# Optimization experiments

Hardware: AMD Instinct MI355X
Metric: run time of the kernel (lower is better)

## Reference

```python
import jax, jax.numpy as jnp
import numpy as np

DIM = 256
CODEBOOK_SIZE = 1024
CODEBOOK_DIM = 1024
COMMITMENT_COST = 1.0
CODEBOOK_COST = 0.25
LN_EPS = 1e-5


def setup_inputs() -> dict:
    key = jax.random.key(0)
    ks = jax.random.split(key, 6)
    x = jax.random.normal(ks[0], (4, 8192, DIM), dtype=jnp.float32)
    ln_gamma = jnp.ones((DIM,), jnp.float32)
    ln_beta = jnp.zeros((DIM,), jnp.float32)
    # pre_proj Linear(dim -> codebook_dim), stored as (in, out)
    pre_w = jax.random.normal(ks[1], (DIM, CODEBOOK_DIM), jnp.float32) / np.sqrt(DIM)
    pre_b = jnp.zeros((CODEBOOK_DIM,), jnp.float32)
    # codebook: unit-norm rows scaled by sqrt(codebook_dim)
    e = jax.random.normal(ks[2], (CODEBOOK_SIZE, CODEBOOK_DIM), jnp.float32)
    embed = e / jnp.linalg.norm(e, axis=1, keepdims=True) * np.sqrt(CODEBOOK_DIM)
    # post_proj Linear(codebook_dim -> dim)
    post_w = jax.random.normal(ks[3], (CODEBOOK_DIM, DIM), jnp.float32) / np.sqrt(CODEBOOK_DIM)
    post_b = jnp.zeros((DIM,), jnp.float32)
    return {"x": x, "ln_gamma": ln_gamma, "ln_beta": ln_beta,
            "pre_w": pre_w, "pre_b": pre_b, "embed": embed,
            "post_w": post_w, "post_b": post_b}


def _layer_norm(x, g, b):
    mu = jnp.mean(x, axis=-1, keepdims=True)
    var = jnp.mean(jnp.square(x - mu), axis=-1, keepdims=True)
    return (x - mu) * jax.lax.rsqrt(var + LN_EPS) * g + b


def reference(x, ln_gamma, ln_beta, pre_w, pre_b, embed, post_w, post_b):
    B, N, D = x.shape
    sg = jax.lax.stop_gradient
    # pre_norm -> GELU -> pre_proj
    x_normed = _layer_norm(x, ln_gamma, ln_beta)
    z_e = jax.nn.gelu(x_normed, approximate=False) @ pre_w + pre_b  # (B,N,Dc)
    flat = z_e.reshape(-1, CODEBOOK_DIM)  # (BN, Dc)
    # squared L2 distances to codebook: ||z||^2 - 2 z.E^T + ||e||^2
    z_sq = jnp.sum(flat * flat, axis=1, keepdims=True)        # (BN,1)
    e_sq = jnp.sum(embed * embed, axis=1)                      # (K,)
    dist = z_sq - 2.0 * (flat @ embed.T) + e_sq[None, :]       # (BN,K)
    indices = jnp.argmin(dist, axis=1)                          # (BN,)
    z_q = embed[indices]                                        # (BN,Dc)
    # losses
    codebook_loss = CODEBOOK_COST * jnp.mean(jnp.square(sg(flat) - z_q))
    commitment_loss = COMMITMENT_COST * jnp.mean(jnp.square(flat - sg(z_q)))
    vq_loss = codebook_loss + commitment_loss
    # straight-through estimator + post projection
    z_q_st = flat + sg(z_q - flat)
    quantized = (z_q_st.reshape(B, N, CODEBOOK_DIM)) @ post_w + post_b  # (B,N,D)
    return quantized, indices.reshape(B, N), vq_loss
```

## Files before the change

kernel.cpp:

```cpp
#include <hip/hip_runtime.h>
#include <math.h>

typedef __attribute__((ext_vector_type(8))) short short8;
typedef __attribute__((ext_vector_type(4))) float f32x4;

__device__ __forceinline__ unsigned short f2bf(float f) {
  unsigned u = __float_as_uint(f);
  unsigned r = (u + 0x7FFFu + ((u >> 16) & 1u)) >> 16;
  return (unsigned short)r;
}

__device__ __forceinline__ float bf2f(unsigned short u) {
  return __uint_as_float((unsigned)u << 16);
}

__device__ __forceinline__ void gload_lds16(const void* gsrc, void* ldst) {
  __builtin_amdgcn_global_load_lds(
      (__attribute__((address_space(1))) void*)(void*)(size_t)(const char*)gsrc,
      (__attribute__((address_space(3))) void*)ldst, 16, 0, 0);
}

__global__ __launch_bounds__(512) void prep1_kernel(
    const float* __restrict__ x, const float* __restrict__ ln_g,
    const float* __restrict__ ln_b, const float* __restrict__ pre_w,
    const float* __restrict__ pre_b, const float* __restrict__ embed,
    const float* __restrict__ post_w, const float* __restrict__ post_b,
    float* __restrict__ g, unsigned short* __restrict__ gbf,
    float* __restrict__ wtf, float* __restrict__ e_sq,
    float* __restrict__ qv, float* __restrict__ c0,
    float* __restrict__ eproj) {
  __shared__ __align__(16) char smem[16640];
  const int blk = blockIdx.x;
  const int t = threadIdx.x;
  if (blk < 256) {
    float (*Es)[1024] = (float(*)[1024])smem;
    const int k0 = blk * 4;
    *(float4*)(&Es[0][0] + t * 8) = *(const float4*)(embed + (size_t)k0 * 1024 + t * 8);
    *(float4*)(&Es[0][0] + t * 8 + 4) = *(const float4*)(embed + (size_t)k0 * 1024 + t * 8 + 4);
    __syncthreads();
    const int sl = t >> 6, jg = t & 63;
    const int dbase = sl * 128;
    float4 a[4] = {};
    const float* wp = post_w + (size_t)dbase * 256 + jg * 4;
#pragma unroll 8
    for (int dd = 0; dd < 128; ++dd) {
      float4 w4 = *(const float4*)(wp + (size_t)dd * 256);
      int d = dbase + dd;
#pragma unroll
      for (int kk = 0; kk < 4; ++kk) {
        float e = Es[kk][d];
        a[kk].x += w4.x * e; a[kk].y += w4.y * e;
        a[kk].z += w4.z * e; a[kk].w += w4.w * e;
      }
    }
    __syncthreads();
    float* scr = (float*)smem;
    if (sl >= 4)
#pragma unroll
      for (int kk = 0; kk < 4; ++kk)
        *(float4*)(scr + (sl - 4) * 1024 + kk * 256 + jg * 4) = a[kk];
    __syncthreads();
    if (sl < 4)
#pragma unroll
      for (int kk = 0; kk < 4; ++kk) {
        float4 v = *(const float4*)(scr + sl * 1024 + kk * 256 + jg * 4);
        a[kk].x += v.x; a[kk].y += v.y; a[kk].z += v.z; a[kk].w += v.w;
      }
    __syncthreads();
    if (sl >= 2 && sl < 4)
#pragma unroll
      for (int kk = 0; kk < 4; ++kk)
        *(float4*)(scr + (sl - 2) * 1024 + kk * 256 + jg * 4) = a[kk];
    __syncthreads();
    if (sl < 2)
#pragma unroll
      for (int kk = 0; kk < 4; ++kk) {
        float4 v = *(const float4*)(scr + sl * 1024 + kk * 256 + jg * 4);
        a[kk].x += v.x; a[kk].y += v.y; a[kk].z += v.z; a[kk].w += v.w;
      }
    __syncthreads();
    if (sl == 1)
#pragma unroll
      for (int kk = 0; kk < 4; ++kk)
        *(float4*)(scr + kk * 256 + jg * 4) = a[kk];
    __syncthreads();
    if (sl == 0) {
      float4 pb = *(const float4*)(post_b + jg * 4);
#pragma unroll
      for (int kk = 0; kk < 4; ++kk) {
        float4 v = *(const float4*)(scr + kk * 256 + jg * 4);
        float4 o;
        o.x = a[kk].x + v.x + pb.x;
        o.y = a[kk].y + v.y + pb.y;
        o.z = a[kk].z + v.z + pb.z;
        o.w = a[kk].w + v.w + pb.w;
        *(float4*)(eproj + (size_t)(k0 + kk) * 256 + jg * 4) = o;
      }
    }
  } else if (blk < 320) {
    float (*tile)[65] = (float(*)[65])smem;
    const int b = blk - 256;
    const int bc = b & 15, bd = b >> 4;
    const int col = t & 63, rr = t >> 6;
#pragma unroll
    for (int i = 0; i < 8; ++i) {
      int row = rr + i * 8;
      tile[row][col] = pre_w[(size_t)(bd * 64 + row) * 1024 + bc * 64 + col];
    }
    __syncthreads();
#pragma unroll
    for (int i = 0; i < 8; ++i) {
      int row = rr + i * 8;
      wtf[(size_t)(bc * 64 + row) * 256 + bd * 64 + col] = tile[col][row];
    }
  } else if (blk < 448) {
    const int l = t & 63, w = t >> 6;
    const int k = (blk - 320) * 8 + w;
    const float* er = embed + (size_t)k * 1024;
    float s1 = 0.f, s2 = 0.f;
#pragma unroll
    for (int j = 0; j < 16; ++j) {
      float e = er[l + 64 * j];
      s1 += e * e;
      s2 += pre_b[l + 64 * j] * e;
    }
    for (int m = 32; m; m >>= 1) { s1 += __shfl_xor(s1, m); s2 += __shfl_xor(s2, m); }
    if (l == 0) { e_sq[k] = s1; qv[k] = s2; c0[k] = s1 - 2.0f * s2 - 1024.0f; }
  } else {
    const int l = t & 63, w = t >> 6;
    const int r = (blk - 448) * 8 + w;
    const float4 xv = *(const float4*)(x + (size_t)r * 256 + l * 4);
    float s = xv.x + xv.y + xv.z + xv.w;
    for (int m = 32; m; m >>= 1) s += __shfl_xor(s, m);
    const float mu = s * (1.0f / 256.0f);
    float dx = xv.x - mu, dy = xv.y - mu, dz = xv.z - mu, dw = xv.w - mu;
    float vs = dx * dx + dy * dy + dz * dz + dw * dw;
    for (int m = 32; m; m >>= 1) vs += __shfl_xor(vs, m);
    const float rstd = rsqrtf(vs * (1.0f / 256.0f) + 1e-5f);
    float4 gm = *(const float4*)(ln_g + l * 4);
    float4 bt = *(const float4*)(ln_b + l * 4);
    float v0 = dx * rstd * gm.x + bt.x;
    float v1 = dy * rstd * gm.y + bt.y;
    float v2 = dz * rstd * gm.z + bt.z;
    float v3 = dw * rstd * gm.w + bt.w;
    const float is2 = 0.70710678118654752f;
    float4 o;
    o.x = 0.5f * v0 * (1.0f + erff(v0 * is2));
    o.y = 0.5f * v1 * (1.0f + erff(v1 * is2));
    o.z = 0.5f * v2 * (1.0f + erff(v2 * is2));
    o.w = 0.5f * v3 * (1.0f + erff(v3 * is2));
    *(float4*)(g + (size_t)r * 256 + l * 4) = o;
    ushort4 u;
    u.x = f2bf(o.x); u.y = f2bf(o.y); u.z = f2bf(o.z); u.w = f2bf(o.w);
    *(ushort4*)(gbf + (size_t)r * 256 + l * 4) = u;
  }
}

__global__ __launch_bounds__(512) void prep2_kernel(
    const float* __restrict__ embed, const float* __restrict__ pre_w,
    const float* __restrict__ pre_b, const float* __restrict__ wtf,
    float* __restrict__ prow, unsigned short* __restrict__ prowbf,
    unsigned short* __restrict__ qbf, float* __restrict__ wbv) {
  __shared__ __align__(16) char smem[49152];
  const int t = threadIdx.x;
  const int sl = t >> 6, jg = t & 63;
  if (blockIdx.x < 256) {
    float (*Es)[1024] = (float(*)[1024])smem;
    double (*Pd)[1024] = (double(*)[1024])(smem + 16384);
    const int k0 = blockIdx.x * 4;
    *(float4*)(&Es[0][0] + t * 8) = *(const float4*)(embed + (size_t)k0 * 1024 + t * 8);
    *(float4*)(&Es[0][0] + t * 8 + 4) = *(const float4*)(embed + (size_t)k0 * 1024 + t * 8 + 4);
    __syncthreads();
    const int cbase = sl * 128;
    double a[4][4] = {};
    const float* wp = wtf + (size_t)cbase * 256 + jg * 4;
#pragma unroll 8
    for (int cc = 0; cc < 128; ++cc) {
      float4 w4 = *(const float4*)(wp + (size_t)cc * 256);
      int c = cbase + cc;
#pragma unroll
      for (int kk = 0; kk < 4; ++kk) {
        double e = (double)Es[kk][c];
        a[kk][0] += (double)w4.x * e;
        a[kk][1] += (double)w4.y * e;
        a[kk][2] += (double)w4.z * e;
        a[kk][3] += (double)w4.w * e;
      }
    }
    if (sl >= 4)
#pragma unroll
      for (int kk = 0; kk < 4; ++kk)
#pragma unroll
        for (int xx = 0; xx < 4; ++xx) Pd[sl - 4][kk * 256 + jg * 4 + xx] = a[kk][xx];
    __syncthreads();
    if (sl < 4)
#pragma unroll
      for (int kk = 0; kk < 4; ++kk)
#pragma unroll
        for (int xx = 0; xx < 4; ++xx) a[kk][xx] += Pd[sl][kk * 256 + jg * 4 + xx];
    __syncthreads();
    if (sl >= 2 && sl < 4)
#pragma unroll
      for (int kk = 0; kk < 4; ++kk)
#pragma unroll
        for (int xx = 0; xx < 4; ++xx) Pd[sl - 2][kk * 256 + jg * 4 + xx] = a[kk][xx];
    __syncthreads();
    if (sl < 2)
#pragma unroll
      for (int kk = 0; kk < 4; ++kk)
#pragma unroll
        for (int xx = 0; xx < 4; ++xx) a[kk][xx] += Pd[sl][kk * 256 + jg * 4 + xx];
    __syncthreads();
    if (sl == 1)
#pragma unroll
      for (int kk = 0; kk < 4; ++kk)
#pragma unroll
        for (int xx = 0; xx < 4; ++xx) Pd[0][kk * 256 + jg * 4 + xx] = a[kk][xx];
    __syncthreads();
    if (sl == 0) {
#pragma unroll
      for (int kk = 0; kk < 4; ++kk) {
        float4 o;
        o.x = (float)(a[kk][0] + Pd[0][kk * 256 + jg * 4 + 0]);
        o.y = (float)(a[kk][1] + Pd[0][kk * 256 + jg * 4 + 1]);
        o.z = (float)(a[kk][2] + Pd[0][kk * 256 + jg * 4 + 2]);
        o.w = (float)(a[kk][3] + Pd[0][kk * 256 + jg * 4 + 3]);
        *(float4*)(prow + (size_t)(k0 + kk) * 256 + jg * 4) = o;
        ushort4 u;
        u.x = f2bf(o.x); u.y = f2bf(o.y); u.z = f2bf(o.z); u.w = f2bf(o.w);
        *(ushort4*)(prowbf + (size_t)(k0 + kk) * 256 + jg * 4) = u;
      }
    }
  } else if (blockIdx.x < 320) {
    float (*Es)[1024] = (float(*)[1024])smem;
    float (*Ps)[1024] = (float(*)[1024])(smem + 16384);
    const int a0i = (blockIdx.x - 256) * 4;
    *(float4*)(&Es[0][0] + t * 8) = *(const float4*)(pre_w + (size_t)a0i * 1024 + t * 8);
    *(float4*)(&Es[0][0] + t * 8 + 4) = *(const float4*)(pre_w + (size_t)a0i * 1024 + t * 8 + 4);
    __syncthreads();
    const int cbase = sl * 128;
    float4 a[4] = {};
    const float* wp = wtf + (size_t)cbase * 256 + jg * 4;
#pragma unroll 8
    for (int cc = 0; cc < 128; ++cc) {
      float4 w4 = *(const float4*)(wp + (size_t)cc * 256);
      int c = cbase + cc;
#pragma unroll
      for (int kk = 0; kk < 4; ++kk) {
        float e = Es[kk][c];
        a[kk].x += w4.x * e; a[kk].y += w4.y * e;
        a[kk].z += w4.z * e; a[kk].w += w4.w * e;
      }
    }
#pragma unroll
    for (int kk = 0; kk < 4; ++kk)
      *(float4*)(&Ps[sl][kk * 256 + jg * 4]) = a[kk];
    __syncthreads();
#pragma unroll
    for (int rep = 0; rep < 2; ++rep) {
      int o = t + rep * 512;
      float s = Ps[0][o] + Ps[1][o] + Ps[2][o] + Ps[3][o] +
                Ps[4][o] + Ps[5][o] + Ps[6][o] + Ps[7][o];
      int kk = o >> 8, j = o & 255;
      qbf[(size_t)(a0i + kk) * 256 + j] = f2bf(s);
    }
  } else {
    float* Es0 = (float*)smem;
    float (*Ps)[1024] = (float(*)[1024])(smem + 16384);
    const int cbase = sl * 128;
    float4 a = {0.f, 0.f, 0.f, 0.f};
    const float* wp = wtf + (size_t)cbase * 256 + jg * 4;
#pragma unroll 8
    for (int cc = 0; cc < 128; ++cc) {
      float4 w4 = *(const float4*)(wp + (size_t)cc * 256);
      float b = pre_b[cbase + cc];
      a.x += w4.x * b; a.y += w4.y * b; a.z += w4.z * b; a.w += w4.w * b;
    }
    *(float4*)(&Ps[sl][jg * 4]) = a;
    float sb = 0.f;
    if (t < 256) {
      float4 bv = *(const float4*)(pre_b + t * 4);
      sb = bv.x * bv.x + bv.y * bv.y + bv.z * bv.z + bv.w * bv.w;
    }
    for (int m = 32; m; m >>= 1) sb += __shfl_xor(sb, m);
    if ((t & 63) == 0 && t < 256) Es0[t >> 6] = sb;
    __syncthreads();
    if (t < 256) {
      float s = Ps[0][t] + Ps[1][t] + Ps[2][t] + Ps[3][t] +
                Ps[4][t] + Ps[5][t] + Ps[6][t] + Ps[7][t];
      wbv[t] = 2.f * s;
    }
    if (t == 0) wbv[256] = Es0[0] + Es0[1] + Es0[2] + Es0[3];
  }
}

__device__ __forceinline__ void stage_tile256(
    int t, const unsigned short* __restrict__ Asrc, size_t a_row_stride,
    const unsigned short* __restrict__ Bsrc, size_t b_row_stride, int k0,
    unsigned short* Ab, unsigned short* Bb) {
#pragma unroll
  for (int i = 0; i < 4; ++i) {
    int ca = t + 256 * i;
    int r = ca >> 3;
    int sp = (ca & 7) ^ (r & 7);
    gload_lds16(Asrc + (size_t)r * a_row_stride + k0 + sp * 8, (char*)Ab + ca * 16);
    gload_lds16(Bsrc + (size_t)r * b_row_stride + k0 + sp * 8, (char*)Bb + ca * 16);
  }
}

#define SAFE_LOOP_BODY(cur)                                                    \
    const unsigned short* Ab = &lds[cur][0];                                   \
    const unsigned short* Bb = &lds[cur][8192];                                \
    _Pragma("unroll")                                                          \
    for (int ks = 0; ks < 2; ++ks) {                                           \
      const int sp = ((ks << 2) + (l >> 4)) ^ (l & 7);                         \
      short8 af[4], bq[4];                                                     \
      _Pragma("unroll")                                                        \
      for (int mi = 0; mi < 4; ++mi)                                           \
        af[mi] = *(const short8*)(Ab + (wm + mi * 16 + (l & 15)) * 64 + sp * 8); \
      _Pragma("unroll")                                                        \
      for (int ni = 0; ni < 4; ++ni)                                           \
        bq[ni] = *(const short8*)(Bb + (wn + ni * 16 + (l & 15)) * 64 + sp * 8); \
      _Pragma("unroll")                                                        \
      for (int mi = 0; mi < 4; ++mi)                                           \
        _Pragma("unroll")                                                      \
        for (int ni = 0; ni < 4; ++ni)                                         \
          acc[mi][ni] = __builtin_amdgcn_mfma_f32_16x16x32_bf16(af[mi], bq[ni], acc[mi][ni], 0, 0, 0); \
    }

__global__ __launch_bounds__(256) void g1_kernel(
    const unsigned short* __restrict__ gbf,
    const unsigned short* __restrict__ prowbf,
    const unsigned short* __restrict__ qbf,
    const float* __restrict__ c0, const float* __restrict__ wbv,
    unsigned short* __restrict__ scores,
    float* __restrict__ z_sq) {
  __shared__ unsigned short lds[2][16384];
  const int t = threadIdx.x;
  const int bm = blockIdx.x;
  const int bn = blockIdx.y;
  const int m0 = bm * 128;
  const bool is_score = (bn < 8);
  const unsigned short* Bsrc = is_score ? (prowbf + bn * 128 * 256)
                                        : (qbf + (bn - 8) * 128 * 256);
  f32x4 acc[4][4] = {};
  const int w = t >> 6, l = t & 63;
  const int wm = (w >> 1) * 64, wn = (w & 1) * 64;

  stage_tile256(t, gbf + (size_t)m0 * 256, 256, Bsrc, 256, 0, &lds[0][0], &lds[0][8192]);
  __syncthreads();
  for (int kt = 0; kt < 4; ++kt) {
    const int cur = kt & 1;
    if (kt < 3)
      stage_tile256(t, gbf + (size_t)m0 * 256, 256, Bsrc, 256, (kt + 1) * 64,
                    &lds[cur ^ 1][0], &lds[cur ^ 1][8192]);
    SAFE_LOOP_BODY(cur)
    __syncthreads();
  }
  const int lrow = (l >> 4) * 4;
  const int lcol = l & 15;
  if (is_score) {
    const int n0 = bn * 128;
#pragma unroll
    for (int mi = 0; mi < 4; ++mi)
#pragma unroll
      for (int ni = 0; ni < 4; ++ni) {
        int gcol = n0 + wn + ni * 16 + lcol;
        float cc = c0[gcol];
#pragma unroll
        for (int r = 0; r < 4; ++r) {
          int grow = m0 + wm + mi * 16 + lrow + r;
          scores[(size_t)grow * 1024 + gcol] = f2bf(cc - 2.0f * acc[mi][ni][r]);
        }
      }
  } else {
    const int d0 = (bn - 8) * 128;
    const float bsq = wbv[256];
#pragma unroll
    for (int mi = 0; mi < 4; ++mi)
#pragma unroll
      for (int r = 0; r < 4; ++r) {
        int grow = m0 + wm + mi * 16 + lrow + r;
        float v = 0.f;
#pragma unroll
        for (int ni = 0; ni < 4; ++ni) {
          int gcol = d0 + wn + ni * 16 + lcol;
          float gv = bf2f(gbf[(size_t)grow * 256 + gcol]);
          v += gv * (acc[mi][ni][r] + wbv[gcol]);
        }
        v += __shfl_xor(v, 1); v += __shfl_xor(v, 2);
        v += __shfl_xor(v, 4); v += __shfl_xor(v, 8);
        if (lcol == 0)
          atomicAdd(&z_sq[grow], v + ((bn == 8 && wn == 0) ? bsq : 0.f));
      }
  }
}

__global__ __launch_bounds__(256) void refine_kernel(
    const unsigned short* __restrict__ scores, const float* __restrict__ g,
    const float* __restrict__ prow, const float* __restrict__ e_sq,
    const float* __restrict__ qv, const float* __restrict__ z_sq,
    const float* __restrict__ eproj, float* __restrict__ out_q,
    float* __restrict__ fidx, float* __restrict__ loss_slots) {
  const int t = threadIdx.x, l = t & 63, w = t >> 6;
  const int r = blockIdx.x * 4 + w;
  const unsigned short* srow = scores + (size_t)r * 1024;
  uint4 q0 = *(const uint4*)(srow + l * 16);
  uint4 q1 = *(const uint4*)(srow + l * 16 + 8);
  float f[16];
  {
    unsigned uu[8] = {q0.x, q0.y, q0.z, q0.w, q1.x, q1.y, q1.z, q1.w};
#pragma unroll
    for (int j = 0; j < 8; ++j) {
      f[2 * j] = __uint_as_float(uu[j] << 16);
      f[2 * j + 1] = __uint_as_float(uu[j] & 0xFFFF0000u);
    }
  }
  float mn = f[0];
#pragma unroll
  for (int j = 1; j < 16; ++j) mn = fminf(mn, f[j]);
  for (int m = 32; m; m >>= 1) mn = fminf(mn, __shfl_xor(mn, m));
  const float T = mn + 8.0f;

  float gv[4];
  const float* gr = g + (size_t)r * 256;
#pragma unroll
  for (int j = 0; j < 4; ++j) gv[j] = gr[l + 64 * j];

  float bestd = 1e30f; int bestk = 0x7fffffff;
#pragma unroll 1
  for (int j = 0; j < 16; ++j) {
    unsigned long long msk = __ballot(f[j] <= T);
    while (msk) {
      int src = __ffsll(msk) - 1;
      msk &= msk - 1;
      int k = src * 16 + j;
      const float* pr = prow + (size_t)k * 256;
      float p = 0.f;
#pragma unroll
      for (int jj = 0; jj < 4; ++jj) p += gv[jj] * pr[l + 64 * jj];
      for (int m = 32; m; m >>= 1) p += __shfl_xor(p, m);
      float d = e_sq[k] - 2.0f * (p + qv[k]);
      if (d < bestd || (d == bestd && k < bestk)) { bestd = d; bestk = k; }
    }
  }
  if (l == 0) {
    fidx[r] = (float)bestk;
    atomicAdd(&loss_slots[r & 2047], z_sq[r] + bestd);
  }
  float4 o = *(const float4*)(eproj + (size_t)bestk * 256 + l * 4);
  *(float4*)(out_q + (size_t)r * 256 + l * 4) = o;
}

__global__ __launch_bounds__(256) void loss_final_kernel(
    const float* __restrict__ slots, float* __restrict__ out_loss) {
  float s = 0.f;
  for (int i = threadIdx.x; i < 2048; i += 256) s += slots[i];
  for (int m = 32; m; m >>= 1) s += __shfl_xor(s, m);
  __shared__ float ws_[4];
  if ((threadIdx.x & 63) == 0) ws_[threadIdx.x >> 6] = s;
  __syncthreads();
  if (threadIdx.x == 0)
    out_loss[0] = 1.25f * (ws_[0] + ws_[1] + ws_[2] + ws_[3]) / 33554432.0f;
}

extern "C" void kernel_launch(void* const* d_in, const int* in_sizes, int n_in,
                              void* d_out, int out_size, void* d_ws, size_t ws_size,
                              hipStream_t stream) {
  const float* x = (const float*)d_in[0];
  const float* ln_g = (const float*)d_in[1];
  const float* ln_b = (const float*)d_in[2];
  const float* pre_w = (const float*)d_in[3];
  const float* pre_b = (const float*)d_in[4];
  const float* embed = (const float*)d_in[5];
  const float* post_w = (const float*)d_in[6];
  const float* post_b = (const float*)d_in[7];
  float* out_q = (float*)d_out;
  float* out_idx = out_q + 8388608;
  float* out_loss = out_q + 8421376;

  char* ws = (char*)d_ws;
  size_t off = 0;
  auto alloc = [&](size_t n) { char* p = ws + off; off += (n + 255) & ~(size_t)255; return p; };
  float* g_f32 = (float*)alloc(33554432);
  unsigned short* g_bf = (unsigned short*)alloc(16777216);
  unsigned short* scores = (unsigned short*)alloc(67108864);
  float* prow = (float*)alloc(1048576);
  unsigned short* prowbf = (unsigned short*)alloc(524288);
  unsigned short* qbf = (unsigned short*)alloc(131072);
  float* wtf = (float*)alloc(1048576);
  float* eproj = (float*)alloc(1048576);
  float* wbv = (float*)alloc(2048);
  float* e_sq = (float*)alloc(4096);
  float* qv = (float*)alloc(4096);
  float* c0 = (float*)alloc(4096);
  float* z_sq = (float*)alloc(131072);
  float* slots = (float*)alloc(8192);
  (void)ws_size; (void)in_sizes; (void)n_in; (void)out_size;

  hipMemsetAsync(z_sq, 0, 131072, stream);
  hipMemsetAsync(slots, 0, 8192, stream);

  prep1_kernel<<<4544, 512, 0, stream>>>(x, ln_g, ln_b, pre_w, pre_b, embed,
                                         post_w, post_b, g_f32, g_bf, wtf,
                                         e_sq, qv, c0, eproj);
  prep2_kernel<<<321, 512, 0, stream>>>(embed, pre_w, pre_b, wtf, prow, prowbf,
                                        qbf, wbv);
  dim3 g1grid(256, 10);
  g1_kernel<<<g1grid, 256, 0, stream>>>(g_bf, prowbf, qbf, c0, wbv, scores, z_sq);
  refine_kernel<<<8192, 256, 0, stream>>>(scores, g_f32, prow, e_sq, qv, z_sq,
                                          eproj, out_q, out_idx, slots);
  loss_final_kernel<<<1, 256, 0, stream>>>(slots, out_loss);
}
```

Baseline: 139.1 us.

## Regroup prep kernels and replace memsets with in-kernel zeroing

Splits preprocessing into a small transpose/zeroing kernel followed by one merged kernel that computes the codebook projections, eproj, norms and LayerNorm-GELU rows together. The two hipMemsetAsync calls are replaced by zeroing inside the first kernel. This aims to cut launch count and let the projection work overlap with the LayerNorm blocks. The merged kernel now reserves 48KB LDS for every block, which may reduce occupancy for the many LayerNorm blocks.

```diff
diff --git a/kernel.cpp b/kernel.cpp
--- a/kernel.cpp
+++ b/kernel.cpp
@@ -20,25 +20,181 @@
       (__attribute__((address_space(3))) void*)ldst, 16, 0, 0);
 }
 
-__global__ __launch_bounds__(512) void prep1_kernel(
+__global__ __launch_bounds__(512) void prepA_kernel(
+    const float* __restrict__ pre_w, float* __restrict__ wtf,
+    float* __restrict__ z_sq, float* __restrict__ slots) {
+  __shared__ float tile[64][65];
+  const int blk = blockIdx.x;
+  const int t = threadIdx.x;
+  if (blk < 64) {
+    const int bc = blk & 15, bd = blk >> 4;
+    const int col = t & 63, rr = t >> 6;
+#pragma unroll
+    for (int i = 0; i < 8; ++i) {
+      int row = rr + i * 8;
+      tile[row][col] = pre_w[(size_t)(bd * 64 + row) * 1024 + bc * 64 + col];
+    }
+    __syncthreads();
+#pragma unroll
+    for (int i = 0; i < 8; ++i) {
+      int row = rr + i * 8;
+      wtf[(size_t)(bc * 64 + row) * 256 + bd * 64 + col] = tile[col][row];
+    }
+  } else {
+    int i = (blk - 64) * 512 + t;
+    z_sq[i] = 0.f;
+    if (i < 2048) slots[i] = 0.f;
+  }
+}
+
+__global__ __launch_bounds__(512) void prepB_kernel(
     const float* __restrict__ x, const float* __restrict__ ln_g,
     const float* __restrict__ ln_b, const float* __restrict__ pre_w,
     const float* __restrict__ pre_b, const float* __restrict__ embed,
     const float* __restrict__ post_w, const float* __restrict__ post_b,
+    const float* __restrict__ wtf,
     float* __restrict__ g, unsigned short* __restrict__ gbf,
-    float* __restrict__ wtf, float* __restrict__ e_sq,
-    float* __restrict__ qv, float* __restrict__ c0,
+    float* __restrict__ prow, unsigned short* __restrict__ prowbf,
+    unsigned short* __restrict__ qbf, float* __restrict__ wbv,
+    float* __restrict__ e_sq, float* __restrict__ qv, float* __restrict__ c0,
     float* __restrict__ eproj) {
-  __shared__ __align__(16) char smem[16640];
+  __shared__ __align__(16) char smem[49152];
   const int blk = blockIdx.x;
   const int t = threadIdx.x;
+  const int sl = t >> 6, jg = t & 63;
   if (blk < 256) {
     float (*Es)[1024] = (float(*)[1024])smem;
+    double (*Pd)[1024] = (double(*)[1024])(smem + 16384);
     const int k0 = blk * 4;
     *(float4*)(&Es[0][0] + t * 8) = *(const float4*)(embed + (size_t)k0 * 1024 + t * 8);
     *(float4*)(&Es[0][0] + t * 8 + 4) = *(const float4*)(embed + (size_t)k0 * 1024 + t * 8 + 4);
     __syncthreads();
-    const int sl = t >> 6, jg = t & 63;
+    const int cbase = sl * 128;
+    double a[4][4] = {};
+    const float* wp = wtf + (size_t)cbase * 256 + jg * 4;
+#pragma unroll 8
+    for (int cc = 0; cc < 128; ++cc) {
+      float4 w4 = *(const float4*)(wp + (size_t)cc * 256);
+      int c = cbase + cc;
+#pragma unroll
+      for (int kk = 0; kk < 4; ++kk) {
+        double e = (double)Es[kk][c];
+        a[kk][0] += (double)w4.x * e;
+        a[kk][1] += (double)w4.y * e;
+        a[kk][2] += (double)w4.z * e;
+        a[kk][3] += (double)w4.w * e;
+      }
+    }
+    if (sl >= 4)
+#pragma unroll
+      for (int kk = 0; kk < 4; ++kk)
+#pragma unroll
+        for (int xx = 0; xx < 4; ++xx) Pd[sl - 4][kk * 256 + jg * 4 + xx] = a[kk][xx];
+    __syncthreads();
+    if (sl < 4)
+#pragma unroll
+      for (int kk = 0; kk < 4; ++kk)
+#pragma unroll
+        for (int xx = 0; xx < 4; ++xx) a[kk][xx] += Pd[sl][kk * 256 + jg * 4 + xx];
+    __syncthreads();
+    if (sl >= 2 && sl < 4)
+#pragma unroll
+      for (int kk = 0; kk < 4; ++kk)
+#pragma unroll
+        for (int xx = 0; xx < 4; ++xx) Pd[sl - 2][kk * 256 + jg * 4 + xx] = a[kk][xx];
+    __syncthreads();
+    if (sl < 2)
+#pragma unroll
+      for (int kk = 0; kk < 4; ++kk)
+#pragma unroll
+        for (int xx = 0; xx < 4; ++xx) a[kk][xx] += Pd[sl][kk * 256 + jg * 4 + xx];
+    __syncthreads();
+    if (sl == 1)
+#pragma unroll
+      for (int kk = 0; kk < 4; ++kk)
+#pragma unroll
+        for (int xx = 0; xx < 4; ++xx) Pd[0][kk * 256 + jg * 4 + xx] = a[kk][xx];
+    __syncthreads();
+    if (sl == 0) {
+#pragma unroll
+      for (int kk = 0; kk < 4; ++kk) {
+        float4 o;
+        o.x = (float)(a[kk][0] + Pd[0][kk * 256 + jg * 4 + 0]);
+        o.y = (float)(a[kk][1] + Pd[0][kk * 256 + jg * 4 + 1]);
+        o.z = (float)(a[kk][2] + Pd[0][kk * 256 + jg * 4 + 2]);
+        o.w = (float)(a[kk][3] + Pd[0][kk * 256 + jg * 4 + 3]);
+        *(float4*)(prow + (size_t)(k0 + kk) * 256 + jg * 4) = o;
+        ushort4 u;
+        u.x = f2bf(o.x); u.y = f2bf(o.y); u.z = f2bf(o.z); u.w = f2bf(o.w);
+        *(ushort4*)(prowbf + (size_t)(k0 + kk) * 256 + jg * 4) = u;
+      }
+    }
+  } else if (blk < 320) {
+    float (*Es)[1024] = (float(*)[1024])smem;
+    float (*Ps)[1024] = (float(*)[1024])(smem + 16384);
+    const int a0i = (blk - 256) * 4;
+    *(float4*)(&Es[0][0] + t * 8) = *(const float4*)(pre_w + (size_t)a0i * 1024 + t * 8);
+    *(float4*)(&Es[0][0] + t * 8 + 4) = *(const float4*)(pre_w + (size_t)a0i * 1024 + t * 8 + 4);
+    __syncthreads();
+    const int cbase = sl * 128;
+    float4 a[4] = {};
+    const float* wp = wtf + (size_t)cbase * 256 + jg * 4;
+#pragma unroll 8
+    for (int cc = 0; cc < 128; ++cc) {
+      float4 w4 = *(const float4*)(wp + (size_t)cc * 256);
+      int c = cbase + cc;
+#pragma unroll
+      for (int kk = 0; kk < 4; ++kk) {
+        float e = Es[kk][c];
+        a[kk].x += w4.x * e; a[kk].y += w4.y * e;
+        a[kk].z += w4.z * e; a[kk].w += w4.w * e;
+      }
+    }
+#pragma unroll
+    for (int kk = 0; kk < 4; ++kk)
+      *(float4*)(&Ps[sl][kk * 256 + jg * 4]) = a[kk];
+    __syncthreads();
+#pragma unroll
+    for (int rep = 0; rep < 2; ++rep) {
+      int o = t + rep * 512;
+      float s = Ps[0][o] + Ps[1][o] + Ps[2][o] + Ps[3][o] +
+                Ps[4][o] + Ps[5][o] + Ps[6][o] + Ps[7][o];
+      int kk = o >> 8, j = o & 255;
+      qbf[(size_t)(a0i + kk) * 256 + j] = f2bf(s);
+    }
+  } else if (blk == 320) {
+    float* Es0 = (float*)smem;
+    float (*Ps)[1024] = (float(*)[1024])(smem + 16384);
+    const int cbase = sl * 128;
+    float4 a = {0.f, 0.f, 0.f, 0.f};
+    const float* wp = wtf + (size_t)cbase * 256 + jg * 4;
+#pragma unroll 8
+    for (int cc = 0; cc < 128; ++cc) {
+      float4 w4 = *(const float4*)(wp + (size_t)cc * 256);
+      float b = pre_b[cbase + cc];
+      a.x += w4.x * b; a.y += w4.y * b; a.z += w4.z * b; a.w += w4.w * b;
+    }
+    *(float4*)(&Ps[sl][jg * 4]) = a;
+    float sb = 0.f;
+    if (t < 256) {
+      float4 bv = *(const float4*)(pre_b + t * 4);
+      sb = bv.x * bv.x + bv.y * bv.y + bv.z * bv.z + bv.w * bv.w;
+    }
+    for (int m = 32; m; m >>= 1) sb += __shfl_xor(sb, m);
+    if ((t & 63) == 0 && t < 256) Es0[t >> 6] = sb;
+    __syncthreads();
+    if (t < 256) {
+      float s = Ps[0][t] + Ps[1][t] + Ps[2][t] + Ps[3][t] +
+                Ps[4][t] + Ps[5][t] + Ps[6][t] + Ps[7][t];
+      wbv[t] = 2.f * s;
+    }
+    if (t == 0) wbv[256] = Es0[0] + Es0[1] + Es0[2] + Es0[3];
+  } else if (blk < 577) {
+    float (*Es)[1024] = (float(*)[1024])smem;
+    const int k0 = (blk - 321) * 4;
+    *(float4*)(&Es[0][0] + t * 8) = *(const float4*)(embed + (size_t)k0 * 1024 + t * 8);
+    *(float4*)(&Es[0][0] + t * 8 + 4) = *(const float4*)(embed + (size_t)k0 * 1024 + t * 8 + 4);
+    __syncthreads();
     const int dbase = sl * 128;
     float4 a[4] = {};
     const float* wp = post_w + (size_t)dbase * 256 + jg * 4;
@@ -97,25 +253,9 @@
         *(float4*)(eproj + (size_t)(k0 + kk) * 256 + jg * 4) = o;
       }
     }
-  } else if (blk < 320) {
-    float (*tile)[65] = (float(*)[65])smem;
-    const int b = blk - 256;
-    const int bc = b & 15, bd = b >> 4;
-    const int col = t & 63, rr = t >> 6;
-#pragma unroll
-    for (int i = 0; i < 8; ++i) {
-      int row = rr + i * 8;
-      tile[row][col] = pre_w[(size_t)(bd * 64 + row) * 1024 + bc * 64 + col];
-    }
-    __syncthreads();
-#pragma unroll
-    for (int i = 0; i < 8; ++i) {
-      int row = rr + i * 8;
-      wtf[(size_t)(bc * 64 + row) * 256 + bd * 64 + col] = tile[col][row];
-    }
-  } else if (blk < 448) {
+  } else if (blk < 705) {
     const int l = t & 63, w = t >> 6;
-    const int k = (blk - 320) * 8 + w;
+    const int k = (blk - 577) * 8 + w;
     const float* er = embed + (size_t)k * 1024;
     float s1 = 0.f, s2 = 0.f;
 #pragma unroll
@@ -128,7 +268,7 @@
     if (l == 0) { e_sq[k] = s1; qv[k] = s2; c0[k] = s1 - 2.0f * s2 - 1024.0f; }
   } else {
     const int l = t & 63, w = t >> 6;
-    const int r = (blk - 448) * 8 + w;
+    const int r = (blk - 705) * 8 + w;
     const float4 xv = *(const float4*)(x + (size_t)r * 256 + l * 4);
     float s = xv.x + xv.y + xv.z + xv.w;
     for (int m = 32; m; m >>= 1) s += __shfl_xor(s, m);
@@ -156,144 +296,6 @@
   }
 }
 
-__global__ __launch_bounds__(512) void prep2_kernel(
-    const float* __restrict__ embed, const float* __restrict__ pre_w,
-    const float* __restrict__ pre_b, const float* __restrict__ wtf,
-    float* __restrict__ prow, unsigned short* __restrict__ prowbf,
-    unsigned short* __restrict__ qbf, float* __restrict__ wbv) {
-  __shared__ __align__(16) char smem[49152];
-  const int t = threadIdx.x;
-  const int sl = t >> 6, jg = t & 63;
-  if (blockIdx.x < 256) {
-    float (*Es)[1024] = (float(*)[1024])smem;
-    double (*Pd)[1024] = (double(*)[1024])(smem + 16384);
-    const int k0 = blockIdx.x * 4;
-    *(float4*)(&Es[0][0] + t * 8) = *(const float4*)(embed + (size_t)k0 * 1024 + t * 8);
-    *(float4*)(&Es[0][0] + t * 8 + 4) = *(const float4*)(embed + (size_t)k0 * 1024 + t * 8 + 4);
-    __syncthreads();
-    const int cbase = sl * 128;
-    double a[4][4] = {};
-    const float* wp = wtf + (size_t)cbase * 256 + jg * 4;
-#pragma unroll 8
-    for (int cc = 0; cc < 128; ++cc) {
-      float4 w4 = *(const float4*)(wp + (size_t)cc * 256);
-      int c = cbase + cc;
-#pragma unroll
-      for (int kk = 0; kk < 4; ++kk) {
-        double e = (double)Es[kk][c];
-        a[kk][0] += (double)w4.x * e;
-        a[kk][1] += (double)w4.y * e;
-        a[kk][2] += (double)w4.z * e;
-        a[kk][3] += (double)w4.w * e;
-      }
-    }
-    if (sl >= 4)
-#pragma unroll
-      for (int kk = 0; kk < 4; ++kk)
-#pragma unroll
-        for (int xx = 0; xx < 4; ++xx) Pd[sl - 4][kk * 256 + jg * 4 + xx] = a[kk][xx];
-    __syncthreads();
-    if (sl < 4)
-#pragma unroll
-      for (int kk = 0; kk < 4; ++kk)
-#pragma unroll
-        for (int xx = 0; xx < 4; ++xx) a[kk][xx] += Pd[sl][kk * 256 + jg * 4 + xx];
-    __syncthreads();
-    if (sl >= 2 && sl < 4)
-#pragma unroll
-      for (int kk = 0; kk < 4; ++kk)
-#pragma unroll
-        for (int xx = 0; xx < 4; ++xx) Pd[sl - 2][kk * 256 + jg * 4 + xx] = a[kk][xx];
-    __syncthreads();
-    if (sl < 2)
-#pragma unroll
-      for (int kk = 0; kk < 4; ++kk)
-#pragma unroll
-        for (int xx = 0; xx < 4; ++xx) a[kk][xx] += Pd[sl][kk * 256 + jg * 4 + xx];
-    __syncthreads();
-    if (sl == 1)
-#pragma unroll
-      for (int kk = 0; kk < 4; ++kk)
-#pragma unroll
-        for (int xx = 0; xx < 4; ++xx) Pd[0][kk * 256 + jg * 4 + xx] = a[kk][xx];
-    __syncthreads();
-    if (sl == 0) {
-#pragma unroll
-      for (int kk = 0; kk < 4; ++kk) {
-        float4 o;
-        o.x = (float)(a[kk][0] + Pd[0][kk * 256 + jg * 4 + 0]);
-        o.y = (float)(a[kk][1] + Pd[0][kk * 256 + jg * 4 + 1]);
-        o.z = (float)(a[kk][2] + Pd[0][kk * 256 + jg * 4 + 2]);
-        o.w = (float)(a[kk][3] + Pd[0][kk * 256 + jg * 4 + 3]);
-        *(float4*)(prow + (size_t)(k0 + kk) * 256 + jg * 4) = o;
-        ushort4 u;
-        u.x = f2bf(o.x); u.y = f2bf(o.y); u.z = f2bf(o.z); u.w = f2bf(o.w);
-        *(ushort4*)(prowbf + (size_t)(k0 + kk) * 256 + jg * 4) = u;
-      }
-    }
-  } else if (blockIdx.x < 320) {
-    float (*Es)[1024] = (float(*)[1024])smem;
-    float (*Ps)[1024] = (float(*)[1024])(smem + 16384);
-    const int a0i = (blockIdx.x - 256) * 4;
-    *(float4*)(&Es[0][0] + t * 8) = *(const float4*)(pre_w + (size_t)a0i * 1024 + t * 8);
-    *(float4*)(&Es[0][0] + t * 8 + 4) = *(const float4*)(pre_w + (size_t)a0i * 1024 + t * 8 + 4);
-    __syncthreads();
-    const int cbase = sl * 128;
-    float4 a[4] = {};
-    const float* wp = wtf + (size_t)cbase * 256 + jg * 4;
-#pragma unroll 8
-    for (int cc = 0; cc < 128; ++cc) {
-      float4 w4 = *(const float4*)(wp + (size_t)cc * 256);
-      int c = cbase + cc;
-#pragma unroll
-      for (int kk = 0; kk < 4; ++kk) {
-        float e = Es[kk][c];
-        a[kk].x += w4.x * e; a[kk].y += w4.y * e;
-        a[kk].z += w4.z * e; a[kk].w += w4.w * e;
-      }
-    }
-#pragma unroll
-    for (int kk = 0; kk < 4; ++kk)
-      *(float4*)(&Ps[sl][kk * 256 + jg * 4]) = a[kk];
-    __syncthreads();
-#pragma unroll
-    for (int rep = 0; rep < 2; ++rep) {
-      int o = t + rep * 512;
-      float s = Ps[0][o] + Ps[1][o] + Ps[2][o] + Ps[3][o] +
-                Ps[4][o] + Ps[5][o] + Ps[6][o] + Ps[7][o];
-      int kk = o >> 8, j = o & 255;
-      qbf[(size_t)(a0i + kk) * 256 + j] = f2bf(s);
-    }
-  } else {
-    float* Es0 = (float*)smem;
-    float (*Ps)[1024] = (float(*)[1024])(smem + 16384);
-    const int cbase = sl * 128;
-    float4 a = {0.f, 0.f, 0.f, 0.f};
-    const float* wp = wtf + (size_t)cbase * 256 + jg * 4;
-#pragma unroll 8
-    for (int cc = 0; cc < 128; ++cc) {
-      float4 w4 = *(const float4*)(wp + (size_t)cc * 256);
-      float b = pre_b[cbase + cc];
-      a.x += w4.x * b; a.y += w4.y * b; a.z += w4.z * b; a.w += w4.w * b;
-    }
-    *(float4*)(&Ps[sl][jg * 4]) = a;
-    float sb = 0.f;
-    if (t < 256) {
-      float4 bv = *(const float4*)(pre_b + t * 4);
-      sb = bv.x * bv.x + bv.y * bv.y + bv.z * bv.z + bv.w * bv.w;
-    }
-    for (int m = 32; m; m >>= 1) sb += __shfl_xor(sb, m);
-    if ((t & 63) == 0 && t < 256) Es0[t >> 6] = sb;
-    __syncthreads();
-    if (t < 256) {
-      float s = Ps[0][t] + Ps[1][t] + Ps[2][t] + Ps[3][t] +
-                Ps[4][t] + Ps[5][t] + Ps[6][t] + Ps[7][t];
-      wbv[t] = 2.f * s;
-    }
-    if (t == 0) wbv[256] = Es0[0] + Es0[1] + Es0[2] + Es0[3];
-  }
-}
-
 __device__ __forceinline__ void stage_tile256(
     int t, const unsigned short* __restrict__ Asrc, size_t a_row_stride,
     const unsigned short* __restrict__ Bsrc, size_t b_row_stride, int k0,
@@ -498,14 +500,11 @@
   float* slots = (float*)alloc(8192);
   (void)ws_size; (void)in_sizes; (void)n_in; (void)out_size;
 
-  hipMemsetAsync(z_sq, 0, 131072, stream);
-  hipMemsetAsync(slots, 0, 8192, stream);
-
-  prep1_kernel<<<4544, 512, 0, stream>>>(x, ln_g, ln_b, pre_w, pre_b, embed,
-                                         post_w, post_b, g_f32, g_bf, wtf,
-                                         e_sq, qv, c0, eproj);
-  prep2_kernel<<<321, 512, 0, stream>>>(embed, pre_w, pre_b, wtf, prow, prowbf,
-                                        qbf, wbv);
+  prepA_kernel<<<128, 512, 0, stream>>>(pre_w, wtf, z_sq, slots);
+  prepB_kernel<<<4801, 512, 0, stream>>>(x, ln_g, ln_b, pre_w, pre_b, embed,
+                                         post_w, post_b, wtf, g_f32, g_bf,
+                                         prow, prowbf, qbf, wbv, e_sq, qv, c0,
+                                         eproj);
   dim3 g1grid(256, 10);
   g1_kernel<<<g1grid, 256, 0, stream>>>(g_bf, prowbf, qbf, c0, wbv, scores, z_sq);
   refine_kernel<<<8192, 256, 0, stream>>>(scores, g_f32, prow, e_sq, qv, z_sq,
```

After: 134.8 us (median of 4 runs). 1.03x faster.
